# Kernel tuning notes

Measured on AMD Instinct MI355X. Metric: run time of the kernel, lower is better.

## Reference

```python
import jax, jax.numpy as jnp
import numpy as np

N_P, N_W, F_IN = 512, 3584, 256
H1, O1 = 8, 32
H2, O2 = 8, 256
BATCH = 1024
NEG_SLOPE = 0.2


def _xavier(key, shape):
    fan_in, fan_out = shape[-2], shape[-1]
    lim = jnp.sqrt(6.0 / (fan_in + fan_out))
    return jax.random.uniform(key, shape, jnp.float32, -lim, lim)


def setup_inputs() -> dict:
    key = jax.random.key(0)
    ks = jax.random.split(key, 16)
    return {
        "input": jax.random.uniform(ks[0], (BATCH, N_W), jnp.float32),
        "pern_feature": jax.random.normal(ks[1], (N_P, F_IN), jnp.float32),
        "word_feature": jax.random.normal(ks[2], (N_W, F_IN), jnp.float32),
        "w1": _xavier(ks[3], (H1, F_IN, O1)),
        "a_src1": _xavier(ks[4], (H1, O1, 1)),
        "a_dst1": _xavier(ks[5], (H1, O1, 1)),
        "b1": jnp.zeros((O1,), jnp.float32),
        "w2": _xavier(ks[6], (H2, F_IN, O2)),
        "a_src2": _xavier(ks[7], (H2, F_IN, 1)),
        "a_dst2": _xavier(ks[8], (H2, F_IN, 1)),
        "b2": jnp.zeros((O2,), jnp.float32),
        "W_fc": _xavier(ks[9], (O2, 5)),
        "b_fc": jnp.zeros((5,), jnp.float32),
        "pern_adj": jax.random.randint(ks[10], (N_P, N_P), 0, 2, jnp.int32),
        "word_pern_adj": jax.random.randint(ks[11], (N_P + N_W, N_P + N_W), 0, 2, jnp.int32),
    }


def gat(h, adj, w, a_src, a_dst, bias):
    # h: [N, f_in], adj: [N, N] int, w: [H, f_in, f_out]
    h_prime = jnp.einsum('nf,hfo->hno', h, w)          # [H, N, O]
    t = jnp.tanh(h_prime)
    s_src = jnp.einsum('hno,hoi->hn', t, a_src)        # [H, N]
    s_dst = jnp.einsum('hno,hoi->hn', t, a_dst)        # [H, N]
    attn = s_src[:, :, None] + s_dst[:, None, :]       # [H, N, N]
    attn = jnp.where(attn >= 0, attn, NEG_SLOPE * attn)  # leaky_relu
    attn = jnp.where(adj[None, :, :] > 0, attn, -jnp.inf)
    attn = jax.nn.softmax(attn, axis=-1)
    out = jnp.einsum('hnm,hmo->hno', attn, h_prime)    # [H, N, O]
    return out + bias


def reference(input, pern_feature, word_feature, w1, a_src1, a_dst1, b1,
              w2, a_src2, a_dst2, b2, W_fc, b_fc, pern_adj, word_pern_adj):
    n_p = pern_feature.shape[0]
    # GAT 1 over personality graph
    h1 = gat(pern_feature, pern_adj, w1, a_src1, a_dst1, b1)       # [H1, n_p, O1]
    hiddn_pp = jnp.transpose(h1, (1, 0, 2)).reshape(n_p, -1)        # [n_p, H1*O1]
    hiddn_pp = jax.nn.elu(hiddn_pp)
    # dropout is identity in eval mode
    hiddn_wp = jnp.concatenate([word_feature, hiddn_pp], axis=0)    # [N, 256]
    h2 = gat(hiddn_wp, word_pern_adj, w2, a_src2, a_dst2, b2)       # [H2, N, O2]
    hiddn_wp2 = h2.mean(axis=0)                                     # [N, O2]
    hiddn_w = hiddn_wp2[:word_feature.shape[0], :]                  # [n_w, O2]
    x = (input @ hiddn_w) / input.sum(axis=1, keepdims=True)        # [B, O2]
    return x @ W_fc + b_fc                                          # [B, 5]
```

## Files before the change

### kernel.cpp

```cpp
#include <hip/hip_runtime.h>
#include <hip/hip_bf16.h>
#include <math.h>

#define NP 512
#define NW 3584
#define NT 4096
#define FIN 256
#define H1 8
#define O1 32
#define H2 8
#define O2 256
#define NEG 0.2f

typedef __attribute__((ext_vector_type(8))) short bf16x8;
typedef __attribute__((ext_vector_type(4))) float f32x4;
typedef __attribute__((ext_vector_type(2))) float v2f;
typedef unsigned long long u64;

__device__ __forceinline__ unsigned short f2bf(float f) {
    unsigned u = __float_as_uint(f);
    unsigned r = (u + 0x7FFF + ((u >> 16) & 1)) >> 16;
    return (unsigned short)r;
}

__device__ __forceinline__ float fast_tanh(float x) {
    float ex = __expf(2.0f * x);
    return 1.0f - 2.0f / (ex + 1.0f);
}

__global__ __launch_bounds__(256) void k_prep(
    const float* __restrict__ wf, const float* __restrict__ pf,
    const float* __restrict__ w1, const float* __restrict__ a_src1,
    const float* __restrict__ a_dst1, const float* __restrict__ w2,
    const float* __restrict__ b2, const float* __restrict__ W_fc,
    const int* __restrict__ wp_adj,
    unsigned short* __restrict__ abf, unsigned short* __restrict__ btbf,
    float* __restrict__ hp1, float* __restrict__ ss1, float* __restrict__ sd1,
    u64* __restrict__ maskT64, float* __restrict__ cvec)
{
    __shared__ float tile[64][65];
    __shared__ float feat[2][FIN];
    __shared__ float red[4][5];
    int blk = blockIdx.x;
    int t = threadIdx.x;
    if (blk < 896) {
        int idx4 = blk * 256 + t;
        float4 x = ((const float4*)wf)[idx4];
        ushort4 y;
        y.x = f2bf(x.x); y.y = f2bf(x.y); y.z = f2bf(x.z); y.w = f2bf(x.w);
        ((ushort4*)abf)[idx4] = y;
    } else if (blk < 1152) {
        int n0 = (blk - 896) * 2;
        feat[0][t] = pf[n0 * FIN + t];
        feat[1][t] = pf[(n0 + 1) * FIN + t];
        __syncthreads();
        int h = t >> 5, o = t & 31;
        float acc0 = 0.f, acc1 = 0.f;
        const float* wcol = w1 + h * FIN * O1 + o;
        #pragma unroll 4
        for (int f = 0; f < FIN; f++) {
            float w = wcol[f * O1];
            acc0 += feat[0][f] * w;
            acc1 += feat[1][f] * w;
        }
        hp1[n0 * 256 + t] = acc0;
        hp1[(n0 + 1) * 256 + t] = acc1;
        float as = a_src1[h * O1 + o];
        float ad = a_dst1[h * O1 + o];
        float accs[2] = {acc0, acc1};
        #pragma unroll
        for (int i = 0; i < 2; i++) {
            float th = tanhf(accs[i]);
            float vs = th * as, vd = th * ad;
            #pragma unroll
            for (int off = 1; off < 32; off <<= 1) {
                vs += __shfl_xor(vs, off);
                vd += __shfl_xor(vd, off);
            }
            if (o == 0) { ss1[h * NP + n0 + i] = vs; sd1[h * NP + n0 + i] = vd; }
        }
    } else if (blk < 1280) {
        int blk2 = blk - 1152;
        int h = blk2 >> 4;
        int f0 = ((blk2 >> 2) & 3) * 64;
        int o0 = (blk2 & 3) * 64;
        #pragma unroll
        for (int rr = 0; rr < 16; rr++) {
            int f = rr * 4 + (t >> 6);
            int o = t & 63;
            tile[f][o] = w2[((size_t)(h * FIN + f0 + f)) * O2 + o0 + o];
        }
        __syncthreads();
        #pragma unroll
        for (int rr = 0; rr < 16; rr++) {
            int o = rr * 4 + (t >> 6);
            int f = t & 63;
            btbf[((size_t)(h * O2 + o0 + o)) * FIN + f0 + f] = f2bf(tile[f][o]);
        }
    } else if (blk < 2176) {
        int w = t >> 6, l = t & 63;
        int r = (blk - 1280) * 4 + w;
        const int4* row = (const int4*)(wp_adj + (size_t)r * NT);
        for (int c4 = 0; c4 < 16; c4++) {
            int4 x = row[c4 * 64 + l];
            u64 nib = (u64)((x.x != 0 ? 1 : 0) | (x.y != 0 ? 2 : 0) |
                            (x.z != 0 ? 4 : 0) | (x.w != 0 ? 8 : 0));
            u64 v = nib << (4 * (l & 15));
            v |= __shfl_xor(v, 1);
            v |= __shfl_xor(v, 2);
            v |= __shfl_xor(v, 4);
            v |= __shfl_xor(v, 8);
            if ((l & 15) == 0) {
                int qw = c4 * 4 + (l >> 4);
                maskT64[(size_t)qw * NW + r] = v;
            }
        }
    } else {
        float v[5];
        #pragma unroll
        for (int j = 0; j < 5; j++) v[j] = b2[t] * W_fc[t * 5 + j];
        #pragma unroll
        for (int off = 1; off < 64; off <<= 1)
            #pragma unroll
            for (int j = 0; j < 5; j++) v[j] += __shfl_xor(v[j], off);
        int w = t >> 6, l = t & 63;
        if (l == 0) { for (int j = 0; j < 5; j++) red[w][j] = v[j]; }
        __syncthreads();
        if (t == 0)
            for (int j = 0; j < 5; j++) cvec[j] = red[0][j] + red[1][j] + red[2][j] + red[3][j];
    }
}

__global__ __launch_bounds__(256) void k_gat1_attn(
    const int* __restrict__ adj, const float* __restrict__ hp1,
    const float* __restrict__ ss1, const float* __restrict__ sd1,
    const float* __restrict__ b1, unsigned short* __restrict__ abf)
{
    __shared__ float p[2][H1][NP];
    __shared__ float den[2][H1];
    int t = threadIdx.x;
    int n0 = blockIdx.x * 2;
    for (int rr = 0; rr < 32; rr++) {
        int idx = rr * 256 + t;
        int i = idx >> 12, h = (idx >> 9) & 7, m = idx & 511;
        float a = adj[(n0 + i) * NP + m] > 0 ? 1.0f : 0.0f;
        float e = ss1[h * NP + n0 + i] + sd1[h * NP + m];
        e = fmaxf(e, NEG * e);
        p[i][h][m] = a * __expf(e);
    }
    __syncthreads();
    int w = t >> 6, l = t & 63;
    {
        int i = w & 1;
        #pragma unroll
        for (int hh = 0; hh < 4; hh++) {
            int h = (w >> 1) * 4 + hh;
            float s = 0;
            #pragma unroll
            for (int q = 0; q < 8; q++) s += p[i][h][l + 64 * q];
            #pragma unroll
            for (int off = 1; off < 64; off <<= 1) s += __shfl_xor(s, off);
            if (l == 0) den[i][h] = s;
        }
    }
    __syncthreads();
    int h = t >> 5, o = t & 31;
    float acc[2] = {0, 0};
    #pragma unroll 4
    for (int m = 0; m < NP; m++) {
        float v = hp1[m * 256 + t];
        acc[0] += p[0][h][m] * v;
        acc[1] += p[1][h][m] * v;
    }
    float bo = b1[o];
    #pragma unroll
    for (int i = 0; i < 2; i++) {
        float r = acc[i] / den[i][h] + bo;
        r = r > 0.f ? r : expm1f(r);
        abf[(NW + n0 + i) * FIN + t] = f2bf(r);
    }
}

__global__ __launch_bounds__(256) void k_gemm_hp2(
    const unsigned short* __restrict__ abf, const unsigned short* __restrict__ btbf,
    const float* __restrict__ a_src2, const float* __restrict__ a_dst2,
    const float* __restrict__ W_fc, float* __restrict__ gpart)
{
    int bid = blockIdx.x;
    int h = bid >> 6;
    int rem = bid & 63;
    int mt = rem >> 1, nt = rem & 1;
    int w = threadIdx.x >> 6, l = threadIdx.x & 63;
    int m0 = mt * 128 + (w >> 1) * 64;
    int n0 = nt * 128 + (w & 1) * 64;
    int lr = l & 15, lq = l >> 4;
    const unsigned short* bbase = btbf + h * O2 * FIN;
    f32x4 acc[4][4];
    #pragma unroll
    for (int i = 0; i < 4; i++)
        #pragma unroll
        for (int j = 0; j < 4; j++) acc[i][j] = (f32x4){0.f, 0.f, 0.f, 0.f};
    for (int k = 0; k < FIN; k += 32) {
        bf16x8 a[4], b[4];
        int kc = k + lq * 8;
        #pragma unroll
        for (int i = 0; i < 4; i++)
            a[i] = *(const bf16x8*)(abf + (m0 + i * 16 + lr) * FIN + kc);
        #pragma unroll
        for (int j = 0; j < 4; j++)
            b[j] = *(const bf16x8*)(bbase + (n0 + j * 16 + lr) * FIN + kc);
        #pragma unroll
        for (int i = 0; i < 4; i++)
            #pragma unroll
            for (int j = 0; j < 4; j++)
                acc[i][j] = __builtin_amdgcn_mfma_f32_16x16x32_bf16(a[i], b[j], acc[i][j], 0, 0, 0);
    }
    int slice = nt * 2 + (w & 1);
    float as[4], ad[4], wfc[4][5];
    #pragma unroll
    for (int j = 0; j < 4; j++) {
        int col = n0 + j * 16 + lr;
        as[j] = a_src2[h * O2 + col];
        ad[j] = a_dst2[h * O2 + col];
        #pragma unroll
        for (int jj = 0; jj < 5; jj++) wfc[j][jj] = W_fc[col * 5 + jj];
    }
    float* base = gpart + ((size_t)h * 4 + slice) * NT * 8;
    #pragma unroll
    for (int i = 0; i < 4; i++) {
        #pragma unroll
        for (int r = 0; r < 4; r++) {
            float s[7] = {0,0,0,0,0,0,0};
            #pragma unroll
            for (int j = 0; j < 4; j++) {
                float x = acc[i][j][r];
                float th = fast_tanh(x);
                s[0] += th * as[j];
                s[1] += th * ad[j];
                #pragma unroll
                for (int jj = 0; jj < 5; jj++) s[2 + jj] += x * wfc[j][jj];
            }
            #pragma unroll
            for (int off = 1; off < 16; off <<= 1)
                #pragma unroll
                for (int q = 0; q < 7; q++) s[q] += __shfl_xor(s[q], off);
            if (lr == 0) {
                int m = m0 + i * 16 + lq * 4 + r;
                float* dst = base + (size_t)m * 8;
                #pragma unroll
                for (int q = 0; q < 7; q++) dst[q] = s[q];
            }
        }
    }
}

__global__ __launch_bounds__(256) void k_comb_hp2(
    const float* __restrict__ gpart,
    float* __restrict__ Etab, float* __restrict__ Eptab, float* __restrict__ T)
{
    int idx = blockIdx.x * 256 + threadIdx.x;
    float s[7] = {0,0,0,0,0,0,0};
    #pragma unroll
    for (int sl = 0; sl < 4; sl++) {
        const float* p = gpart + (((size_t)(idx >> 12) * 4 + sl) * NT + (idx & (NT - 1))) * 8;
        #pragma unroll
        for (int q = 0; q < 7; q++) s[q] += p[q];
    }
    Etab[idx]  = __expf(s[0]);
    Eptab[idx] = __expf(NEG * s[0]);
    float4 t0 = {__expf(s[1]), __expf(NEG * s[1]), 1.0f, s[2]};
    float4 t1 = {s[3], s[4], s[5], s[6]};
    *(float4*)(T + (size_t)idx * 8)     = t0;
    *(float4*)(T + (size_t)idx * 8 + 4) = t1;
}

__global__ __launch_bounds__(256) void k_gat2_attn(
    const u64* __restrict__ maskT64, const float* __restrict__ Etab,
    const float* __restrict__ Eptab, const float* __restrict__ T,
    float* __restrict__ part)
{
    int t = threadIdx.x;
    int w = t >> 6, l = t & 63;
    int b = blockIdx.x;
    int nb = b % 112;
    int h  = (b / 112) & 7;
    int c  = b / 896;
    int n0 = __builtin_amdgcn_readfirstlane(nb * 32 + w * 8);
    u64 epk[8];
    #pragma unroll
    for (int i = 0; i < 8; i++) {
        int r = h * NT + n0 + i;
        unsigned e  = __builtin_amdgcn_readfirstlane(__float_as_uint(Etab[r]));
        unsigned ep = __builtin_amdgcn_readfirstlane(__float_as_uint(Eptab[r]));
        epk[i] = ((u64)ep << 32) | e;
    }
    float den[8] = {0,0,0,0,0,0,0,0};
    float num[8][5] = {{0}};
    const float* Th = T + ((size_t)h * NT + c * 2048) * 8;
    for (int q = 0; q < 32; q++) {
        const float* tp = Th + (size_t)(q * 64 + l) * 8;
        f32x4 t0 = *(const f32x4*)tp;
        f32x4 t1 = *(const f32x4*)(tp + 4);
        v2f ffp = {t0.x, t0.y};
        size_t moff = (size_t)(c * 32 + q) * NW + n0;
        const u64* mq = maskT64 + moff;
        #pragma unroll
        for (int i = 0; i < 8; i++) {
            u64 wv = mq[i];
            unsigned wlo = __builtin_amdgcn_readfirstlane((unsigned)wv);
            unsigned whi = __builtin_amdgcn_readfirstlane((unsigned)(wv >> 32));
            u64 word = ((u64)whi << 32) | wlo;
            v2f pab;
            asm("v_pk_mul_f32 %0, %1, %2" : "=v"(pab) : "v"(ffp), "s"(epk[i]));
            float pp0 = fmaxf(pab.x, pab.y);
            float pp;
            asm("v_cndmask_b32 %0, 0, %1, %2" : "=v"(pp) : "v"(pp0), "s"(word));
            den[i] += pp;
            num[i][0] = fmaf(pp, t0.w, num[i][0]);
            num[i][1] = fmaf(pp, t1.x, num[i][1]);
            num[i][2] = fmaf(pp, t1.y, num[i][2]);
            num[i][3] = fmaf(pp, t1.z, num[i][3]);
            num[i][4] = fmaf(pp, t1.w, num[i][4]);
        }
    }
    #pragma unroll
    for (int i = 0; i < 8; i++) {
        float v[6];
        v[0] = den[i];
        #pragma unroll
        for (int j = 0; j < 5; j++) v[1 + j] = num[i][j];
        #pragma unroll
        for (int off = 1; off < 8; off <<= 1)
            #pragma unroll
            for (int k = 0; k < 6; k++) v[k] += __shfl_xor(v[k], off);
        if ((l & 7) == 0) {
            float* dst = part + ((((size_t)c * NW + n0 + i) * 8 + h) * 8 + (l >> 3)) * 8;
            #pragma unroll
            for (int k = 0; k < 6; k++) dst[k] = v[k];
        }
    }
}

__global__ __launch_bounds__(256) void k_gat2_comb(const float* __restrict__ part,
                                                   float* __restrict__ hf) {
    int idx = blockIdx.x * 256 + threadIdx.x;
    int n = idx >> 3, h = idx & 7;
    float den = 0, num[5] = {0,0,0,0,0};
    #pragma unroll
    for (int cc = 0; cc < 2; cc++) {
        #pragma unroll
        for (int s = 0; s < 8; s++) {
            const float* p = part + ((((size_t)cc * NW + n) * 8 + h) * 8 + s) * 8;
            float4 a = *(const float4*)p;
            float4 bq = *(const float4*)(p + 4);
            den += a.x;
            num[0] += a.y; num[1] += a.z; num[2] += a.w;
            num[3] += bq.x; num[4] += bq.y;
        }
    }
    float inv = 1.0f / (den * 8.0f);
    float v[5];
    #pragma unroll
    for (int j = 0; j < 5; j++) v[j] = num[j] * inv;
    #pragma unroll
    for (int off = 1; off < 8; off <<= 1)
        #pragma unroll
        for (int j = 0; j < 5; j++) v[j] += __shfl_xor(v[j], off);
    if (h == 0) {
        #pragma unroll
        for (int j = 0; j < 5; j++) hf[n * 5 + j] = v[j];
    }
}

__global__ __launch_bounds__(256) void k_final(
    const float* __restrict__ input, const float* __restrict__ hf,
    const float* __restrict__ cvec, const float* __restrict__ b_fc,
    float* __restrict__ out)
{
    int b = blockIdx.x, t = threadIdx.x;
    const float4* row4 = (const float4*)(input + (size_t)b * NW);
    const float4* hf4 = (const float4*)hf;
    float s = 0.f, a[5] = {0.f, 0.f, 0.f, 0.f, 0.f};
    for (int idx = t; idx < NW / 4; idx += 256) {
        float4 x = row4[idx];
        float f[20];
        #pragma unroll
        for (int q = 0; q < 5; q++) *(float4*)(f + 4 * q) = hf4[idx * 5 + q];
        s += x.x + x.y + x.z + x.w;
        #pragma unroll
        for (int j = 0; j < 5; j++)
            a[j] += x.x * f[j] + x.y * f[5 + j] + x.z * f[10 + j] + x.w * f[15 + j];
    }
    #pragma unroll
    for (int off = 1; off < 64; off <<= 1) {
        s += __shfl_xor(s, off);
        #pragma unroll
        for (int j = 0; j < 5; j++) a[j] += __shfl_xor(a[j], off);
    }
    __shared__ float red[4][6];
    int w = t >> 6, l = t & 63;
    if (l == 0) { red[w][0] = s; for (int j = 0; j < 5; j++) red[w][j + 1] = a[j]; }
    __syncthreads();
    if (t < 5) {
        float st = red[0][0] + red[1][0] + red[2][0] + red[3][0];
        float aj = red[0][t + 1] + red[1][t + 1] + red[2][t + 1] + red[3][t + 1];
        out[b * 5 + t] = aj / st + cvec[t] + b_fc[t];
    }
}

extern "C" void kernel_launch(void* const* d_in, const int* in_sizes, int n_in,
                              void* d_out, int out_size, void* d_ws, size_t ws_size,
                              hipStream_t stream) {
    const float* input   = (const float*)d_in[0];
    const float* pf      = (const float*)d_in[1];
    const float* wf      = (const float*)d_in[2];
    const float* w1      = (const float*)d_in[3];
    const float* a_src1  = (const float*)d_in[4];
    const float* a_dst1  = (const float*)d_in[5];
    const float* b1      = (const float*)d_in[6];
    const float* w2      = (const float*)d_in[7];
    const float* a_src2  = (const float*)d_in[8];
    const float* a_dst2  = (const float*)d_in[9];
    const float* b2      = (const float*)d_in[10];
    const float* W_fc    = (const float*)d_in[11];
    const float* b_fc    = (const float*)d_in[12];
    const int* pern_adj  = (const int*)d_in[13];
    const int* wp_adj    = (const int*)d_in[14];
    float* out = (float*)d_out;

    char* ws = (char*)d_ws;
    unsigned short* abf    = (unsigned short*)(ws);
    unsigned short* btbf   = (unsigned short*)(ws + 2097152);
    float*          hp1    = (float*)(ws + 3145728);
    float*          ss1    = (float*)(ws + 3670016);
    float*          sd1    = (float*)(ws + 3686400);
    float*          Etab   = (float*)(ws + 3833856);
    float*          Eptab  = (float*)(ws + 3964928);
    float*          T      = (float*)(ws + 4096000);
    float*          hf     = (float*)(ws + 5144576);
    float*          cvec   = (float*)(ws + 5216256);
    u64*            maskT64= (u64*)(ws + 5216512);
    float*          gpart  = (float*)(ws + 7051520);
    float*          part   = (float*)(ws + 11245824);

    k_prep<<<2177, 256, 0, stream>>>(wf, pf, w1, a_src1, a_dst1, w2, b2, W_fc,
                                     wp_adj, abf, btbf, hp1, ss1, sd1, maskT64, cvec);
    k_gat1_attn<<<256, 256, 0, stream>>>(pern_adj, hp1, ss1, sd1, b1, abf);
    k_gemm_hp2<<<512, 256, 0, stream>>>(abf, btbf, a_src2, a_dst2, W_fc, gpart);
    k_comb_hp2<<<128, 256, 0, stream>>>(gpart, Etab, Eptab, T);
    k_gat2_attn<<<1792, 256, 0, stream>>>(maskT64, Etab, Eptab, T, part);
    k_gat2_comb<<<112, 256, 0, stream>>>(part, hf);
    k_final<<<1024, 256, 0, stream>>>(input, hf, cvec, b_fc, out);
}
```

Measured before the change: 274.4 us.

## Stage A tile in LDS, reorder GEMM blocks, and split GAT1 accumulators

The hp2 GEMM now loads the 128x256 A tile into padded shared memory once per block and reads A fragments from LDS, while B is still read from global memory. Block indexing is reordered so consecutive blocks share the same m-tile across heads and n-tiles, which should improve L2 reuse of A. The GAT1 aggregation loop is unrolled by two with independent accumulators to shorten FMA dependency chains. In exchange the GEMM uses about 66KB of LDS per block, which may limit occupancy, and it adds a barrier before the MFMA loop.

After: 239.9 us. 12.6% less time.

```diff
diff --git a/kernel.cpp b/kernel.cpp
--- a/kernel.cpp
+++ b/kernel.cpp
@@ -165,13 +165,17 @@
     }
     __syncthreads();
     int h = t >> 5, o = t & 31;
-    float acc[2] = {0, 0};
-    #pragma unroll 4
-    for (int m = 0; m < NP; m++) {
-        float v = hp1[m * 256 + t];
-        acc[0] += p[0][h][m] * v;
-        acc[1] += p[1][h][m] * v;
-    }
+    float a0a = 0.f, a0b = 0.f, a1a = 0.f, a1b = 0.f;
+    #pragma unroll 8
+    for (int m = 0; m < NP; m += 2) {
+        float v0 = hp1[m * 256 + t];
+        float v1 = hp1[(m + 1) * 256 + t];
+        a0a += p[0][h][m] * v0;
+        a1a += p[1][h][m] * v0;
+        a0b += p[0][h][m + 1] * v1;
+        a1b += p[1][h][m + 1] * v1;
+    }
+    float acc[2] = {a0a + a0b, a1a + a1b};
     float bo = b1[o];
     #pragma unroll
     for (int i = 0; i < 2; i++) {
@@ -186,12 +190,22 @@
     const float* __restrict__ a_src2, const float* __restrict__ a_dst2,
     const float* __restrict__ W_fc, float* __restrict__ gpart)
 {
-    int bid = blockIdx.x;
-    int h = bid >> 6;
-    int rem = bid & 63;
-    int mt = rem >> 1, nt = rem & 1;
-    int w = threadIdx.x >> 6, l = threadIdx.x & 63;
-    int m0 = mt * 128 + (w >> 1) * 64;
+    __shared__ unsigned short As[128][264];
+    int b = blockIdx.x;
+    int nt = b & 1, h = (b >> 1) & 7, mt = b >> 4;
+    int t = threadIdx.x;
+    int w = t >> 6, l = t & 63;
+    int m0 = mt * 128;
+    {
+        int row = t >> 5;
+        int col8 = (t & 31) * 8;
+        #pragma unroll
+        for (int u = 0; u < 16; u++)
+            *(bf16x8*)(&As[u * 8 + row][col8]) =
+                *(const bf16x8*)(abf + (size_t)(m0 + u * 8 + row) * FIN + col8);
+    }
+    __syncthreads();
+    int am0 = (w >> 1) * 64;
     int n0 = nt * 128 + (w & 1) * 64;
     int lr = l & 15, lq = l >> 4;
     const unsigned short* bbase = btbf + h * O2 * FIN;
@@ -200,20 +214,21 @@
     for (int i = 0; i < 4; i++)
         #pragma unroll
         for (int j = 0; j < 4; j++) acc[i][j] = (f32x4){0.f, 0.f, 0.f, 0.f};
+    #pragma unroll
     for (int k = 0; k < FIN; k += 32) {
-        bf16x8 a[4], b[4];
+        bf16x8 a[4], bf[4];
         int kc = k + lq * 8;
         #pragma unroll
+        for (int j = 0; j < 4; j++)
+            bf[j] = *(const bf16x8*)(bbase + (size_t)(n0 + j * 16 + lr) * FIN + kc);
+        #pragma unroll
         for (int i = 0; i < 4; i++)
-            a[i] = *(const bf16x8*)(abf + (m0 + i * 16 + lr) * FIN + kc);
-        #pragma unroll
-        for (int j = 0; j < 4; j++)
-            b[j] = *(const bf16x8*)(bbase + (n0 + j * 16 + lr) * FIN + kc);
+            a[i] = *(const bf16x8*)(&As[am0 + i * 16 + lr][kc]);
         #pragma unroll
         for (int i = 0; i < 4; i++)
             #pragma unroll
             for (int j = 0; j < 4; j++)
-                acc[i][j] = __builtin_amdgcn_mfma_f32_16x16x32_bf16(a[i], b[j], acc[i][j], 0, 0, 0);
+                acc[i][j] = __builtin_amdgcn_mfma_f32_16x16x32_bf16(a[i], bf[j], acc[i][j], 0, 0, 0);
     }
     int slice = nt * 2 + (w & 1);
     float as[4], ad[4], wfc[4][5];
@@ -245,7 +260,7 @@
                 #pragma unroll
                 for (int q = 0; q < 7; q++) s[q] += __shfl_xor(s[q], off);
             if (lr == 0) {
-                int m = m0 + i * 16 + lq * 4 + r;
+                int m = m0 + am0 + i * 16 + lq * 4 + r;
                 float* dst = base + (size_t)m * 8;
                 #pragma unroll
                 for (int q = 0; q < 7; q++) dst[q] = s[q];
```
